# Kernel tuning notes

Hardware: AMD Instinct MI355X
Metric: run time of the kernel (lower is better)

## Reference

```python
import jax, jax.numpy as jnp
import numpy as np
from jax import lax


def conv3d(x, w, b):
    # x: [B,C,H,W,D], w: [O,I,kh,kw,kd], SAME padding (matches padding=k//2 for odd k)
    out = lax.conv_general_dilated(
        x, w, window_strides=(1, 1, 1), padding='SAME',
        dimension_numbers=('NCDHW', 'OIDHW', 'NCDHW'))
    return out + b[None, :, None, None, None]


def setup_inputs() -> dict:
    key = jax.random.key(0)
    ks = jax.random.split(key, 9)
    B, C, H, W, D = 2, 64, 16, 16, 16
    P = 64  # pab_channels
    s = 0.05
    return {
        'x': jax.random.normal(ks[0], (B, C, H, W, D), jnp.float32),
        'top_w': jax.random.normal(ks[1], (P, C, 1, 1, 1), jnp.float32) * s,
        'top_b': jax.random.normal(ks[2], (P,), jnp.float32) * s,
        'center_w': jax.random.normal(ks[3], (P, C, 1, 1, 1), jnp.float32) * s,
        'center_b': jax.random.normal(ks[4], (P,), jnp.float32) * s,
        'bottom_w': jax.random.normal(ks[5], (C, C, 3, 3, 3), jnp.float32) * s,
        'bottom_b': jax.random.normal(ks[6], (C,), jnp.float32) * s,
        'out_w': jax.random.normal(ks[7], (C, C, 3, 3, 3), jnp.float32) * s,
        'out_b': jax.random.normal(ks[8], (C,), jnp.float32) * s,
    }


def reference(x, top_w, top_b, center_w, center_b, bottom_w, bottom_b, out_w, out_b):
    B, C, H, W, D = x.shape
    N = H * W * D
    x_top = conv3d(x, top_w, top_b).reshape(B, -1, N)            # [B,P,N]
    x_center = conv3d(x, center_w, center_b).reshape(B, -1, N)   # [B,P,N]
    x_bottom = conv3d(x, bottom_w, bottom_b).reshape(B, C, N)    # [B,C,N]
    # sp_map[b,n,m] = sum_p center[b,p,n] * top[b,p,m]
    sp = jnp.einsum('bpn,bpm->bnm', x_center, x_top)             # [B,N,N]
    # GLOBAL softmax over the entire flattened NxN map per batch element
    sp = jax.nn.softmax(sp.reshape(B, N * N), axis=1).reshape(B, N, N)
    sp = jnp.einsum('bnm,bcm->bnc', sp, x_bottom)                # [B,N,C]
    # faithful to torch: plain reshape [B,N,C] -> [B,C,H,W,D] (no transpose)
    sp = sp.reshape(B, C, H, W, D)
    return conv3d(x + sp, out_w, out_b)
```

## Files before the change

### kernel.cpp

```cpp
#include <hip/hip_runtime.h>


typedef __attribute__((ext_vector_type(8))) short bf16x8;
typedef __attribute__((ext_vector_type(4))) short short4v;
typedef __attribute__((ext_vector_type(4))) float f32x4;

#define DEVI static __device__ __forceinline__

DEVI f32x4 MFMA16(bf16x8 a, bf16x8 b, f32x4 c) {
  return __builtin_amdgcn_mfma_f32_16x16x32_bf16(a, b, c, 0, 0, 0);
}
DEVI f32x4 zero4() { return (f32x4){0.f, 0.f, 0.f, 0.f}; }

DEVI unsigned short f2bf(float f) {
  unsigned u = __float_as_uint(f);
  return (unsigned short)((u + 0x7fffu + ((u >> 16) & 1u)) >> 16);
}
DEVI float bf2f(unsigned short u) { return __uint_as_float((unsigned)u << 16); }
DEVI float fexp2(float x) { return __builtin_amdgcn_exp2f(x); }

DEVI unsigned cvtpk(float lo, float hi) {
  unsigned d;
  asm("v_cvt_pk_bf16_f32 %0, %1, %2" : "=v"(d) : "v"(lo), "v"(hi));
  return d;
}
DEVI bf16x8 pack8(f32x4 a, f32x4 b) {
  union { unsigned u[4]; bf16x8 v; } r;
  r.u[0] = cvtpk(a[0], a[1]);
  r.u[1] = cvtpk(a[2], a[3]);
  r.u[2] = cvtpk(b[0], b[1]);
  r.u[3] = cvtpk(b[2], b[3]);
  return r.v;
}

DEVI void gll16(const unsigned short* g, unsigned short* l) {
  __builtin_amdgcn_global_load_lds(
      (const __attribute__((address_space(1))) void*)g,
      (__attribute__((address_space(3))) void*)l, 16, 0, 0);
}

DEVI int permM(int n) {
  return (n & ~63) | (n & 32) | ((n & 12) << 1) | ((n & 16) >> 2) | (n & 3);
}

__global__ void k_prep(const float* __restrict__ tw, const float* __restrict__ cw,
                       const float* __restrict__ bw, const float* __restrict__ ow,
                       const float* __restrict__ x,
                       unsigned short* __restrict__ wkTopF, unsigned short* __restrict__ wkCenF,
                       unsigned short* __restrict__ wkBotF, unsigned short* __restrict__ wkOutF,
                       unsigned short* __restrict__ xT, unsigned short* __restrict__ zbuf) {
  __shared__ float tile[64][65];
  int bx = blockIdx.x;
  int tid = threadIdx.x;
  if (bx == 0 && tid < 64) zbuf[tid] = 0;
  if (bx < 432) {
    int t = bx * 256 + tid;
    if (t < 4096) {
      int co = t >> 6, ci = t & 63;
      int cog = co >> 4, col = co & 15, kc = ci >> 5, kg = (ci & 31) >> 3, e = ci & 7;
      int dst = (((cog * 2 + kc) * 64) + col + 16 * kg) * 8 + e;
      wkTopF[dst] = f2bf(tw[t]);
      wkCenF[dst] = f2bf(cw[t]);
    }
    int k = t % 27;
    int ci = (t / 27) & 63;
    int co = t / (27 * 64);
    int cog = co >> 4, col = co & 15, kc = ci >> 5, kg = (ci & 31) >> 3, e = ci & 7;
    int dst = ((((cog * 27 + k) * 2 + kc) * 64) + col + 16 * kg) * 8 + e;
    wkBotF[dst] = f2bf(bw[t]);
    wkOutF[dst] = f2bf(ow[t]);
    return;
  }
  int bx2 = bx - 432;
  int b = bx2 >> 6;
  int n0 = (bx2 & 63) << 6;
  {
    int nl = tid & 63, cq = tid >> 6;
    const float* xb = x + (size_t)b * 262144;
#pragma unroll
    for (int j = 0; j < 16; j++) {
      int c = cq * 16 + j;
      tile[c][nl] = xb[(size_t)c * 4096 + n0 + nl];
    }
  }
  __syncthreads();
  {
    int n = tid >> 2, c0 = (tid & 3) << 4;
    bf16x8 o0, o1;
#pragma unroll
    for (int j = 0; j < 8; j++) {
      o0[j] = (short)f2bf(tile[c0 + j][n]);
      o1[j] = (short)f2bf(tile[c0 + 8 + j][n]);
    }
    unsigned short* dst = xT + ((size_t)(b * 4096 + n0 + n)) * 64 + c0;
    *(bf16x8*)(dst) = o0;
    *(bf16x8*)(dst + 8) = o1;
  }
}

template <int OMODE>
DEVI void conv3_body(int bx, int t,
                     const unsigned short* __restrict__ wkF,
                     const unsigned short* __restrict__ xTb,
                     const float* __restrict__ bias,
                     const unsigned short* __restrict__ zbuf,
                     float* __restrict__ outF, unsigned short* __restrict__ outH,
                     unsigned short* hl) {
  int ch = bx & 1, wp = (bx >> 1) & 7, h = (bx >> 4) & 15, b = bx >> 8;
  int lane = t & 63, w = t >> 6;
  int col = lane & 15, kg = lane >> 4;
  const unsigned short* xb = xTb + (size_t)b * 262144;
  int row8 = lane >> 3, blk = lane & 7;
#pragma unroll
  for (int q = 0; q < 6; q++) {
    int vi0 = w * 48 + q * 8;
    int vi = vi0 + row8;
    int dhv = vi >> 6, wv = (vi >> 4) & 3, dv = vi & 15;
    int hh = h + dhv - 1, ww = wp * 2 + wv - 1;
    bool val = ((unsigned)hh < 16u) & ((unsigned)ww < 16u);
    int sw = blk ^ (vi & 7);
    const unsigned short* src =
        val ? (xb + ((size_t)((hh * 256 + ww * 16 + dv)) << 6) + sw * 8) : (zbuf + blk * 8);
    gll16(src, hl + vi0 * 64);
  }
  __syncthreads();
  int wi = w & 1;
  int kc = w >> 1;
  const char* hlb = (const char*)hl;
  f32x4 acc0 = zero4(), acc1 = zero4();
#pragma unroll
  for (int k = 0; k < 27; k++) {
    const int dh = k / 9;
    const int dw = (k / 3) % 3;
    const int dz = k % 3 - 1;
    int dsum = col + dz;
    bool vd = (unsigned)dsum < 16u;
    int dcl = vd ? dsum : col;
    int sv = dh * 64 + (wi + dw) * 16 + dcl;
    int g = (kc * 4 + kg) ^ (sv & 7);
    bf16x8 bv = *(const bf16x8*)(hlb + sv * 128 + g * 16);
    if (!vd) bv = (bf16x8){0, 0, 0, 0, 0, 0, 0, 0};
    bf16x8 av0 = *(const bf16x8*)(wkF + (((size_t)((2 * ch) * 27 + k) * 2 + kc) << 9) + lane * 8);
    bf16x8 av1 = *(const bf16x8*)(wkF + (((size_t)((2 * ch + 1) * 27 + k) * 2 + kc) << 9) + lane * 8);
    acc0 = MFMA16(av0, bv, acc0);
    acc1 = MFMA16(av1, bv, acc1);
  }
  __syncthreads();
  f32x4* red = (f32x4*)hl;
  if (kc == 1) {
    red[(wi * 2 + 0) * 64 + lane] = acc0;
    red[(wi * 2 + 1) * 64 + lane] = acc1;
  }
  __syncthreads();
  if (kc == 0) {
    acc0 += red[(wi * 2 + 0) * 64 + lane];
    acc1 += red[(wi * 2 + 1) * 64 + lane];
    int n0c = h * 256 + (wp * 2 + wi) * 16 + col;
    int nst = (OMODE == 2) ? permM(n0c) : n0c;
#pragma unroll
    for (int cgi = 0; cgi < 2; cgi++) {
#pragma unroll
      for (int r = 0; r < 4; r++) {
        int co = (ch * 2 + cgi) * 16 + kg * 4 + r;
        float v = (cgi ? acc1[r] : acc0[r]) + bias[co];
        if (OMODE == 2)
          outH[(size_t)(b * 64 + co) * 4096 + nst] = f2bf(v);
        else
          outF[(size_t)(b * 64 + co) * 4096 + nst] = v;
      }
    }
  }
}

__global__ __launch_bounds__(256, 2) void k_convA(
    const unsigned short* __restrict__ wkTf, const unsigned short* __restrict__ wkCf,
    const unsigned short* __restrict__ wkBf, const unsigned short* __restrict__ xTb,
    const float* __restrict__ tbias, const float* __restrict__ cbias,
    const float* __restrict__ bbias, const unsigned short* __restrict__ zbuf,
    unsigned short* __restrict__ topT, unsigned short* __restrict__ cenT,
    unsigned short* __restrict__ botS) {
  __shared__ __align__(16) unsigned short hl[192 * 64];
  int bx0 = blockIdx.x;
  int t = threadIdx.x;
  if (bx0 >= 512) {
    conv3_body<2>(bx0 - 512, t, wkBf, xTb, bbias, zbuf, nullptr, botS, hl);
    return;
  }
  int lane = t & 63, wid = t >> 6;
  int col = lane & 15, kg = lane >> 4;
  int bx = bx0;
  int b = bx >> 8;
  int rest = bx & 255;
  int nt = rest >> 1, ch = rest & 1;
  int cg = ch * 2 + (wid >> 1);
  int co0 = ch * 32 + (wid >> 1) * 16;
  int n0c = nt * 32 + (wid & 1) * 16 + col;
  const unsigned short* xb = xTb + (size_t)b * 262144;
  f32x4 aT0 = zero4(), aT1 = zero4(), aC0 = zero4(), aC1 = zero4();
#pragma unroll
  for (int kc = 0; kc < 2; kc++) {
    bf16x8 bv = *(const bf16x8*)(xb + (size_t)n0c * 64 + kc * 32 + kg * 8);
    bf16x8 avT = *(const bf16x8*)(wkTf + (((size_t)cg * 2 + kc) * 64 + lane) * 8);
    bf16x8 avC = *(const bf16x8*)(wkCf + (((size_t)cg * 2 + kc) * 64 + lane) * 8);
    if (kc == 0) {
      aT0 = MFMA16(avT, bv, aT0);
      aC0 = MFMA16(avC, bv, aC0);
    } else {
      aT1 = MFMA16(avT, bv, aT1);
      aC1 = MFMA16(avC, bv, aC1);
    }
  }
  const float LOG2E = 1.4426950408889634f;
  short4v sT, sC;
#pragma unroll
  for (int r = 0; r < 4; r++) {
    float bvT = tbias[co0 + kg * 4 + r];
    float bvC = cbias[co0 + kg * 4 + r];
    sT[r] = (short)f2bf(aT0[r] + aT1[r] + bvT);
    sC[r] = (short)f2bf((aC0[r] + aC1[r] + bvC) * LOG2E);
  }
  size_t o = (size_t)(b * 4096 + n0c) * 64 + co0 + kg * 4;
  *(short4v*)(topT + o) = sT;
  *(short4v*)(cenT + o) = sC;
}

__global__ __launch_bounds__(256, 2) void k_convOut(
    const unsigned short* __restrict__ wkOf, const unsigned short* __restrict__ xTb,
    const float* __restrict__ bias, const unsigned short* __restrict__ zbuf,
    float* __restrict__ outF) {
  __shared__ __align__(16) unsigned short hl[192 * 64];
  conv3_body<1>(blockIdx.x, threadIdx.x, wkOf, xTb, bias, zbuf, outF, nullptr, hl);
}

__global__ __launch_bounds__(256, 2) void k_pass2(
    const unsigned short* __restrict__ cenT, const unsigned short* __restrict__ topT,
    const unsigned short* __restrict__ botS,
    unsigned short* __restrict__ part, float* __restrict__ Zpart) {
  __shared__ __align__(16) unsigned short topS[2][4096];
  __shared__ __align__(16) unsigned short botL[2][4096];
  __shared__ float zred[4];
  int bx = blockIdx.x;
  int b = bx >> 8;
  int ntp = (bx >> 3) & 31;
  int mc = bx & 7;
  int t = threadIdx.x;
  int lane = t & 63, w = t >> 6;
  int col = lane & 15, kg = lane >> 4;
  const unsigned short* cb = cenT + (size_t)b * 262144;
  const unsigned short* tb = topT + (size_t)b * 262144;
  const unsigned short* bb = botS + (size_t)b * 262144;
  int nA = ntp * 128 + w * 16;
  int mcBase = mc * 512;
  int row8 = lane >> 3, blk = lane & 7;
  int sw = blk ^ (row8 & 7);

  bf16x8 aA0 = *(const bf16x8*)(cb + (size_t)(nA + col) * 64 + kg * 8);
  bf16x8 aA1 = *(const bf16x8*)(cb + (size_t)(nA + col) * 64 + 32 + kg * 8);
  bf16x8 aB0 = *(const bf16x8*)(cb + (size_t)(nA + 64 + col) * 64 + kg * 8);
  bf16x8 aB1 = *(const bf16x8*)(cb + (size_t)(nA + 64 + col) * 64 + 32 + kg * 8);

  if (w < 2) {
#pragma unroll
    for (int q = 0; q < 4; q++) {
      int s = w * 4 + q;
      gll16(tb + (size_t)(mcBase + s * 8 + row8) * 64 + sw * 8, &topS[0][s * 512]);
    }
  } else {
#pragma unroll
    for (int q = 0; q < 4; q++) {
      int s = (w - 2) * 4 + q;
      gll16(bb + (size_t)(s * 8 + row8) * 4096 + mcBase + sw * 8, &botL[0][s * 512]);
    }
  }

  f32x4 accOA[4], accOB[4];
#pragma unroll
  for (int ct = 0; ct < 4; ct++) {
    accOA[ct] = zero4();
    accOB[ct] = zero4();
  }
  float zs = 0.f;
  int swc = (col & 7) << 3;

  for (int j = 0; j < 8; j++) {
    int cur = j & 1;
    if (j < 7) {
      int m0n = mcBase + (j + 1) * 64;
      if (w < 2) {
#pragma unroll
        for (int q = 0; q < 4; q++) {
          int s = w * 4 + q;
          gll16(tb + (size_t)(m0n + s * 8 + row8) * 64 + sw * 8, &topS[cur ^ 1][s * 512]);
        }
      } else {
#pragma unroll
        for (int q = 0; q < 4; q++) {
          int s = (w - 2) * 4 + q;
          gll16(bb + (size_t)(s * 8 + row8) * 4096 + m0n + sw * 8, &botL[cur ^ 1][s * 512]);
        }
      }
      asm volatile("s_waitcnt vmcnt(4)" ::: "memory");
    } else {
      asm volatile("s_waitcnt vmcnt(0)" ::: "memory");
    }
    __builtin_amdgcn_s_barrier();
    f32x4 sA[4], sB[4];
#pragma unroll
    for (int mt = 0; mt < 4; mt++) {
      bf16x8 b0 = *(const bf16x8*)&topS[cur][(mt * 16 + col) * 64 + ((kg * 8) ^ swc)];
      bf16x8 b1 = *(const bf16x8*)&topS[cur][(mt * 16 + col) * 64 + ((32 + kg * 8) ^ swc)];
      sA[mt] = MFMA16(b1, aA1, MFMA16(b0, aA0, zero4()));
      sB[mt] = MFMA16(b1, aB1, MFMA16(b0, aB0, zero4()));
    }
#pragma unroll
    for (int mt = 0; mt < 4; mt++)
#pragma unroll
      for (int r = 0; r < 4; r++) {
        sA[mt][r] = fexp2(sA[mt][r]);
        sB[mt][r] = fexp2(sB[mt][r]);
        zs += sA[mt][r] + sB[mt][r];
      }
#pragma unroll
    for (int kc = 0; kc < 2; kc++) {
      bf16x8 paA = pack8(sA[2 * kc], sA[2 * kc + 1]);
      bf16x8 paB = pack8(sB[2 * kc], sB[2 * kc + 1]);
#pragma unroll
      for (int ct = 0; ct < 4; ct++) {
        bf16x8 bv = *(const bf16x8*)&botL[cur][(ct * 16 + col) * 64 + ((kc * 32 + kg * 8) ^ swc)];
        accOA[ct] = MFMA16(paA, bv, accOA[ct]);
        accOB[ct] = MFMA16(paB, bv, accOB[ct]);
      }
    }
  }
  unsigned short* po = part + (((size_t)(b * 8 + mc) * 4096 + nA) << 6);
#pragma unroll
  for (int ct = 0; ct < 4; ct++)
#pragma unroll
    for (int r = 0; r < 4; r++) {
      po[(kg * 4 + r) * 64 + ct * 16 + col] = f2bf(accOA[ct][r]);
      po[(64 + kg * 4 + r) * 64 + ct * 16 + col] = f2bf(accOB[ct][r]);
    }
#pragma unroll
  for (int off = 32; off; off >>= 1) zs += __shfl_xor(zs, off);
  if (lane == 0) zred[w] = zs;
  __syncthreads();
  if (t == 0) Zpart[b * 256 + ntp * 8 + mc] = zred[0] + zred[1] + zred[2] + zred[3];
}

__global__ void k_xt1(const float* __restrict__ x, const unsigned short* __restrict__ part,
                      const float* __restrict__ Zpart, unsigned short* __restrict__ xT) {
  __shared__ float tile[64][65];
  __shared__ float zr[4];
  int bx = blockIdx.x;
  int b = bx >> 6;
  int n0 = (bx & 63) << 6;
  int t = threadIdx.x;
  float zv = Zpart[b * 256 + t];
#pragma unroll
  for (int off = 32; off; off >>= 1) zv += __shfl_xor(zv, off);
  if ((t & 63) == 0) zr[t >> 6] = zv;
  __syncthreads();
  float invZ = 1.0f / (zr[0] + zr[1] + zr[2] + zr[3]);
  {
    int c = t >> 2, nl16 = (t & 3) << 4;
    int nt6 = n0 >> 6;
    float acc[16];
#pragma unroll
    for (int k = 0; k < 16; k++) acc[k] = 0.f;
#pragma unroll
    for (int mcq = 0; mcq < 8; mcq++) {
      const unsigned short* pp =
          part + (((size_t)(b * 8 + mcq) * 4096) + c * 64 + nt6) * 64 + nl16;
      bf16x8 v0 = *(const bf16x8*)pp;
      bf16x8 v1 = *(const bf16x8*)(pp + 8);
#pragma unroll
      for (int k = 0; k < 8; k++) {
        acc[k] += bf2f((unsigned short)v0[k]);
        acc[8 + k] += bf2f((unsigned short)v1[k]);
      }
    }
    const float* xb = x + (size_t)b * 262144 + (size_t)c * 4096 + n0 + nl16;
#pragma unroll
    for (int q = 0; q < 4; q++) {
      f32x4 xv = *(const f32x4*)(xb + q * 4);
#pragma unroll
      for (int k = 0; k < 4; k++) tile[c][nl16 + q * 4 + k] = xv[k] + acc[q * 4 + k] * invZ;
    }
  }
  __syncthreads();
  {
    int n = t >> 2, c0 = (t & 3) << 4;
    bf16x8 o0, o1;
#pragma unroll
    for (int j = 0; j < 8; j++) {
      o0[j] = (short)f2bf(tile[c0 + j][n]);
      o1[j] = (short)f2bf(tile[c0 + 8 + j][n]);
    }
    unsigned short* dst = xT + ((size_t)(b * 4096 + n0 + n)) * 64 + c0;
    *(bf16x8*)(dst) = o0;
    *(bf16x8*)(dst + 8) = o1;
  }
}

extern "C" void kernel_launch(void* const* d_in, const int* in_sizes, int n_in,
                              void* d_out, int out_size, void* d_ws, size_t ws_size,
                              hipStream_t stream) {
  const float* x = (const float*)d_in[0];
  const float* tw = (const float*)d_in[1];
  const float* tb = (const float*)d_in[2];
  const float* cw = (const float*)d_in[3];
  const float* cbb = (const float*)d_in[4];
  const float* bw = (const float*)d_in[5];
  const float* bb = (const float*)d_in[6];
  const float* ow = (const float*)d_in[7];
  const float* ob = (const float*)d_in[8];
  float* out = (float*)d_out;
  char* ws = (char*)d_ws;

  unsigned short* wkTopF = (unsigned short*)(ws + 0);
  unsigned short* wkCenF = (unsigned short*)(ws + 8192);
  unsigned short* wkBotF = (unsigned short*)(ws + 16384);
  unsigned short* wkOutF = (unsigned short*)(ws + 237568);
  unsigned short* xT = (unsigned short*)(ws + 458752);
  unsigned short* topT = (unsigned short*)(ws + 1507328);
  unsigned short* cenT = (unsigned short*)(ws + 2555904);
  unsigned short* botS = (unsigned short*)(ws + 3604480);
  unsigned short* yT = (unsigned short*)(ws + 4653056);
  unsigned short* part = (unsigned short*)(ws + 5701632);
  float* Zpart = (float*)(ws + 14090240);
  unsigned short* zbuf = (unsigned short*)(ws + 14092288);

  k_prep<<<560, 256, 0, stream>>>(tw, cw, bw, ow, x, wkTopF, wkCenF, wkBotF, wkOutF, xT, zbuf);
  k_convA<<<1024, 256, 0, stream>>>(wkTopF, wkCenF, wkBotF, xT, tb, cbb, bb, zbuf, topT, cenT, botS);
  k_pass2<<<512, 256, 0, stream>>>(cenT, topT, botS, part, Zpart);
  k_xt1<<<128, 256, 0, stream>>>(x, part, Zpart, yT);
  k_convOut<<<512, 256, 0, stream>>>(wkOutF, yT, ob, zbuf, out);
}
```

Baseline: 44.02 us.

## Triple-buffer pass2 LDS tiles and software-pipeline score MFMAs ahead of exp

Moves the attention pass2 kernel from double to triple LDS buffering with a prefetch distance of two tiles, and fully unrolls the tile loop. The score MFMAs for tile j+1 are issued before the PV MFMAs of tile j, so exp and pack work can overlap matrix math. The aim is to hide global-load latency and the exp dependency chain. In exchange, LDS use per block grows from 32KB to 48KB and register pressure rises from the extra score accumulators, which could limit the 2-blocks-per-SIMD occupancy target.

```diff
diff --git a/kernel.cpp b/kernel.cpp
--- a/kernel.cpp
+++ b/kernel.cpp
@@ -236,8 +236,8 @@
     const unsigned short* __restrict__ cenT, const unsigned short* __restrict__ topT,
     const unsigned short* __restrict__ botS,
     unsigned short* __restrict__ part, float* __restrict__ Zpart) {
-  __shared__ __align__(16) unsigned short topS[2][4096];
-  __shared__ __align__(16) unsigned short botL[2][4096];
+  __shared__ __align__(16) unsigned short topS[3][4096];
+  __shared__ __align__(16) unsigned short botL[3][4096];
   __shared__ float zred[4];
   int bx = blockIdx.x;
   int b = bx >> 8;
@@ -259,19 +259,40 @@
   bf16x8 aB0 = *(const bf16x8*)(cb + (size_t)(nA + 64 + col) * 64 + kg * 8);
   bf16x8 aB1 = *(const bf16x8*)(cb + (size_t)(nA + 64 + col) * 64 + 32 + kg * 8);
 
-  if (w < 2) {
-#pragma unroll
-    for (int q = 0; q < 4; q++) {
-      int s = w * 4 + q;
-      gll16(tb + (size_t)(mcBase + s * 8 + row8) * 64 + sw * 8, &topS[0][s * 512]);
-    }
-  } else {
-#pragma unroll
-    for (int q = 0; q < 4; q++) {
-      int s = (w - 2) * 4 + q;
-      gll16(bb + (size_t)(s * 8 + row8) * 4096 + mcBase + sw * 8, &botL[0][s * 512]);
-    }
-  }
+#define STAGE_TILE(TILE, BUF)                                                         \
+  do {                                                                                \
+    int m0_ = mcBase + (TILE) * 64;                                                   \
+    if (w < 2) {                                                                      \
+      _Pragma("unroll") for (int q = 0; q < 4; q++) {                                 \
+        int s_ = w * 4 + q;                                                           \
+        gll16(tb + (size_t)(m0_ + s_ * 8 + row8) * 64 + sw * 8, &topS[BUF][s_ * 512]); \
+      }                                                                               \
+    } else {                                                                          \
+      _Pragma("unroll") for (int q = 0; q < 4; q++) {                                 \
+        int s_ = (w - 2) * 4 + q;                                                     \
+        gll16(bb + (size_t)(s_ * 8 + row8) * 4096 + m0_ + sw * 8, &botL[BUF][s_ * 512]); \
+      }                                                                               \
+    }                                                                                 \
+  } while (0)
+
+  int swc = (col & 7) << 3;
+#define COMPS(BUF, SA, SB)                                                             \
+  do {                                                                                 \
+    _Pragma("unroll") for (int mt = 0; mt < 4; mt++) {                                 \
+      bf16x8 b0 = *(const bf16x8*)&topS[BUF][(mt * 16 + col) * 64 + ((kg * 8) ^ swc)]; \
+      bf16x8 b1 = *(const bf16x8*)&topS[BUF][(mt * 16 + col) * 64 + ((32 + kg * 8) ^ swc)]; \
+      SA[mt] = MFMA16(b1, aA1, MFMA16(b0, aA0, zero4()));                              \
+      SB[mt] = MFMA16(b1, aB1, MFMA16(b0, aB0, zero4()));                              \
+    }                                                                                  \
+  } while (0)
+
+  STAGE_TILE(0, 0);
+  STAGE_TILE(1, 1);
+  asm volatile("s_waitcnt vmcnt(4)" ::: "memory");
+  __builtin_amdgcn_s_barrier();
+
+  f32x4 sA[4], sB[4], nAx[4], nBx[4];
+  COMPS(0, sA, sB);
 
   f32x4 accOA[4], accOB[4];
 #pragma unroll
@@ -280,38 +301,10 @@
     accOB[ct] = zero4();
   }
   float zs = 0.f;
-  int swc = (col & 7) << 3;
-
+
+#pragma unroll
   for (int j = 0; j < 8; j++) {
-    int cur = j & 1;
-    if (j < 7) {
-      int m0n = mcBase + (j + 1) * 64;
-      if (w < 2) {
-#pragma unroll
-        for (int q = 0; q < 4; q++) {
-          int s = w * 4 + q;
-          gll16(tb + (size_t)(m0n + s * 8 + row8) * 64 + sw * 8, &topS[cur ^ 1][s * 512]);
-        }
-      } else {
-#pragma unroll
-        for (int q = 0; q < 4; q++) {
-          int s = (w - 2) * 4 + q;
-          gll16(bb + (size_t)(s * 8 + row8) * 4096 + m0n + sw * 8, &botL[cur ^ 1][s * 512]);
-        }
-      }
-      asm volatile("s_waitcnt vmcnt(4)" ::: "memory");
-    } else {
-      asm volatile("s_waitcnt vmcnt(0)" ::: "memory");
-    }
-    __builtin_amdgcn_s_barrier();
-    f32x4 sA[4], sB[4];
-#pragma unroll
-    for (int mt = 0; mt < 4; mt++) {
-      bf16x8 b0 = *(const bf16x8*)&topS[cur][(mt * 16 + col) * 64 + ((kg * 8) ^ swc)];
-      bf16x8 b1 = *(const bf16x8*)&topS[cur][(mt * 16 + col) * 64 + ((32 + kg * 8) ^ swc)];
-      sA[mt] = MFMA16(b1, aA1, MFMA16(b0, aA0, zero4()));
-      sB[mt] = MFMA16(b1, aB1, MFMA16(b0, aB0, zero4()));
-    }
+    const int cur = j % 3;
 #pragma unroll
     for (int mt = 0; mt < 4; mt++)
 #pragma unroll
@@ -320,10 +313,20 @@
         sB[mt][r] = fexp2(sB[mt][r]);
         zs += sA[mt][r] + sB[mt][r];
       }
+    bf16x8 paA0 = pack8(sA[0], sA[1]);
+    bf16x8 paA1 = pack8(sA[2], sA[3]);
+    bf16x8 paB0 = pack8(sB[0], sB[1]);
+    bf16x8 paB1 = pack8(sB[2], sB[3]);
+    if (j < 7) {
+      asm volatile("s_waitcnt vmcnt(0)" ::: "memory");
+      __builtin_amdgcn_s_barrier();
+      if (j < 6) STAGE_TILE(j + 2, (j + 2) % 3);
+      COMPS((j + 1) % 3, nAx, nBx);
+    }
 #pragma unroll
     for (int kc = 0; kc < 2; kc++) {
-      bf16x8 paA = pack8(sA[2 * kc], sA[2 * kc + 1]);
-      bf16x8 paB = pack8(sB[2 * kc], sB[2 * kc + 1]);
+      bf16x8 paA = kc ? paA1 : paA0;
+      bf16x8 paB = kc ? paB1 : paB0;
 #pragma unroll
       for (int ct = 0; ct < 4; ct++) {
         bf16x8 bv = *(const bf16x8*)&botL[cur][(ct * 16 + col) * 64 + ((kc * 32 + kg * 8) ^ swc)];
@@ -331,7 +334,16 @@
         accOB[ct] = MFMA16(paB, bv, accOB[ct]);
       }
     }
-  }
+    if (j < 7) {
+#pragma unroll
+      for (int mt = 0; mt < 4; mt++) {
+        sA[mt] = nAx[mt];
+        sB[mt] = nBx[mt];
+      }
+    }
+  }
+#undef STAGE_TILE
+#undef COMPS
   unsigned short* po = part + (((size_t)(b * 8 + mc) * 4096 + nA) << 6);
 #pragma unroll
   for (int ct = 0; ct < 4; ct++)
```

New measurement: 48.72 us. +10.7%, slower.
